# Performance work log

Measured on AMD Instinct MI355X. Metric: run time of the kernel, lower is better.

Reference implementation:

```python
import jax, jax.numpy as jnp
import numpy as np

B, S, D, H, FF = 2, 4096, 1024, 16, 4096
HD = D // H


def _layernorm(x, g, b, eps=1e-5):
    mu = jnp.mean(x, axis=-1, keepdims=True)
    var = jnp.var(x, axis=-1, keepdims=True)
    return (x - mu) * jax.lax.rsqrt(var + eps) * g + b


def setup_inputs() -> dict:
    key = jax.random.key(0)
    ks = jax.random.split(key, 20)
    sd = 1.0 / np.sqrt(D)
    sf = 1.0 / np.sqrt(FF)
    inp = {
        "x": jax.random.normal(ks[0], (B, S, D), jnp.float32),
        # attention projections, stored as [in, out]
        "wq": jax.random.normal(ks[1], (D, D), jnp.float32) * sd,
        "bq": jnp.zeros((D,), jnp.float32),
        "wk": jax.random.normal(ks[2], (D, D), jnp.float32) * sd,
        "bk": jnp.zeros((D,), jnp.float32),
        "wv": jax.random.normal(ks[3], (D, D), jnp.float32) * sd,
        "bv": jnp.zeros((D,), jnp.float32),
        "wo": jax.random.normal(ks[4], (D, D), jnp.float32) * sd,
        "bo": jnp.zeros((D,), jnp.float32),
        # block norm1 (pre-attention)
        "ln1_g": jnp.ones((D,), jnp.float32),
        "ln1_b": jnp.zeros((D,), jnp.float32),
        # FFN internal norm
        "lnf_g": jnp.ones((D,), jnp.float32),
        "lnf_b": jnp.zeros((D,), jnp.float32),
        # gated FFN
        "w1": jax.random.normal(ks[5], (D, FF), jnp.float32) * sd,
        "b1": jnp.zeros((FF,), jnp.float32),
        "wg": jax.random.normal(ks[6], (D, FF), jnp.float32) * sd,
        "bg": jnp.zeros((FF,), jnp.float32),
        "w2": jax.random.normal(ks[7], (FF, D), jnp.float32) * sf,
        "b2": jnp.zeros((D,), jnp.float32),
    }
    return inp


def reference(x, wq, bq, wk, bk, wv, bv, wo, bo, ln1_g, ln1_b,
              lnf_g, lnf_b, w1, b1, wg, bg, w2, b2):
    # pre-norm attention
    residual = x
    h = _layernorm(x, ln1_g, ln1_b)
    q = (h @ wq + bq).reshape(B, S, H, HD).transpose(0, 2, 1, 3)  # [B,H,S,hd]
    k = (h @ wk + bk).reshape(B, S, H, HD).transpose(0, 2, 1, 3)
    v = (h @ wv + bv).reshape(B, S, H, HD).transpose(0, 2, 1, 3)
    scores = jnp.einsum("bhqd,bhkd->bhqk", q, k) / np.sqrt(HD)
    attn = jax.nn.softmax(scores, axis=-1)  # [B,H,S,S] materialized as in torch src
    ctx = jnp.einsum("bhqk,bhkd->bhqd", attn, v)
    ctx = ctx.transpose(0, 2, 1, 3).reshape(B, S, D)
    attn_out = ctx @ wo + bo
    x = residual + attn_out  # dropout = 0 (eval)

    # gated FFN with internal pre-norm and residual
    res2 = x
    h2 = _layernorm(x, lnf_g, lnf_b)
    gate = jax.nn.sigmoid(h2 @ wg + bg)
    up = jax.nn.gelu(h2 @ w1 + b1, approximate=False)
    out = (up * gate) @ w2 + b2
    return out + res2
```

## Files before the change

### kernel.cpp

```cpp
#include <hip/hip_runtime.h>
#include <hip/hip_bf16.h>

#define BB 2
#define SS 4096
#define DD 1024
#define HH 16
#define HD 64
#define FF 4096
#define MM (BB*SS)

typedef __hip_bfloat16 bf16;
typedef __attribute__((ext_vector_type(8))) __bf16 v8bf;
typedef __attribute__((ext_vector_type(4))) float f32x4;
typedef __attribute__((ext_vector_type(16))) float f32x16;
typedef __attribute__((ext_vector_type(8))) unsigned short u16v8;

__device__ __forceinline__ f32x4 mfma16(v8bf a, v8bf b, f32x4 c) {
  return __builtin_amdgcn_mfma_f32_16x16x32_bf16(a, b, c, 0, 0, 0);
}
__device__ __forceinline__ f32x16 mfma32(v8bf a, v8bf b, f32x16 c) {
  return __builtin_amdgcn_mfma_f32_32x32x16_bf16(a, b, c, 0, 0, 0);
}
__device__ __forceinline__ void gload16(const void* g, void* l) {
  __builtin_amdgcn_global_load_lds((const __attribute__((address_space(1))) void*)g,
                                   (__attribute__((address_space(3))) void*)l, 16, 0, 0);
}
__device__ __forceinline__ unsigned cvtpk_bf16(float lo, float hi) {
  unsigned r;
  asm("v_cvt_pk_bf16_f32 %0, %1, %2" : "=v"(r) : "v"(lo), "v"(hi));
  return r;
}

__global__ void k_tcvt(const float* __restrict__ W, bf16* __restrict__ Wt, int K, int N)
{
  __shared__ float tile[32][33];
  const int n0 = blockIdx.x * 32, k0 = blockIdx.y * 32;
  const int tx = threadIdx.x, ty = threadIdx.y;
#pragma unroll
  for (int i = 0; i < 32; i += 8)
    tile[ty + i][tx] = W[(long)(k0 + ty + i) * N + n0 + tx];
  __syncthreads();
#pragma unroll
  for (int i = 0; i < 32; i += 8)
    Wt[(long)(n0 + ty + i) * K + k0 + tx] = __float2bfloat16(tile[tx][ty + i]);
}

__global__ __launch_bounds__(256)
void k_vtrans(const bf16* __restrict__ V, bf16* __restrict__ Vt)
{
  __shared__ bf16 tile[64][72];
  const int s0 = blockIdx.x * 64;
  const int h  = blockIdx.y;
  const int b  = blockIdx.z;
  const int t  = threadIdx.x;
  const int r = t >> 3, c8 = t & 7;
#pragma unroll
  for (int it = 0; it < 2; ++it) {
    const int sr = it * 32 + r;
    const u16v8 v = *(const u16v8*)(V + (long)(b * SS + s0 + sr) * DD + h * 64 + c8 * 8);
#pragma unroll
    for (int e = 0; e < 8; ++e)
      ((unsigned short*)&tile[sr][0])[c8 * 8 + e] = v[e];
  }
  __syncthreads();
#pragma unroll
  for (int it = 0; it < 2; ++it) {
    const int d = it * 32 + r;
    union { unsigned short s[8]; u16v8 v; } o;
#pragma unroll
    for (int e = 0; e < 8; ++e)
      o.s[e] = ((const unsigned short*)tile)[(c8 * 8 + e) * 72 + d];
    *(u16v8*)(Vt + ((long)(b * HH + h) * HD + d) * (long)SS + s0 + c8 * 8) = o.v;
  }
}

__global__ __launch_bounds__(256)
void k_layernorm(const float* __restrict__ x, const float* __restrict__ g,
                 const float* __restrict__ b, bf16* __restrict__ out)
{
  const int row = blockIdx.x;
  const float4 v = ((const float4*)(x + (long)row * DD))[threadIdx.x];
  float s  = v.x + v.y + v.z + v.w;
  float s2 = v.x*v.x + v.y*v.y + v.z*v.z + v.w*v.w;
#pragma unroll
  for (int off = 1; off < 64; off <<= 1) {
    s  += __shfl_xor(s,  off);
    s2 += __shfl_xor(s2, off);
  }
  __shared__ float red[8];
  if ((threadIdx.x & 63) == 0) {
    red[threadIdx.x >> 6]       = s;
    red[(threadIdx.x >> 6) + 4] = s2;
  }
  __syncthreads();
  s  = red[0] + red[1] + red[2] + red[3];
  s2 = red[4] + red[5] + red[6] + red[7];
  const float mu = s * (1.f / DD);
  const float rs = rsqrtf(s2 * (1.f / DD) - mu * mu + 1e-5f);
  const float4 gv = ((const float4*)g)[threadIdx.x];
  const float4 bv = ((const float4*)b)[threadIdx.x];
  bf16* op = out + (long)row * DD + threadIdx.x * 4;
  op[0] = __float2bfloat16((v.x - mu) * rs * gv.x + bv.x);
  op[1] = __float2bfloat16((v.y - mu) * rs * gv.y + bv.y);
  op[2] = __float2bfloat16((v.z - mu) * rs * gv.z + bv.z);
  op[3] = __float2bfloat16((v.w - mu) * rs * gv.w + bv.w);
}

template<int EPI>
__global__ __launch_bounds__(256, 2)
void k_gemm(const bf16* __restrict__ A, const bf16* __restrict__ Bt,
            const float* __restrict__ bias, const float* __restrict__ res,
            void* __restrict__ Cout, int M, int N, int K, float scale)
{
  __shared__ __align__(16) bf16 As[128 * 32];
  __shared__ __align__(16) bf16 Bs[128 * 32];
  const int t = threadIdx.x;
  const int lane = t & 63, w = t >> 6;
  const int wr = w >> 1, wc = w & 1;
  const int fr = lane & 15, fq = lane >> 4;
  const long m0 = (long)blockIdx.y * 128, n0 = (long)blockIdx.x * 128;

  f32x4 acc[4][4] = {};

  const bf16* Ag0 = A  + (m0 + (t >> 2)) * K + (t & 3) * 8;
  const bf16* Ag1 = Ag0 + 64L * K;
  const bf16* Bg0 = Bt + (n0 + (t >> 2)) * K + (t & 3) * 8;
  const bf16* Bg1 = Bg0 + 64L * K;
  bf16* Al0 = As + t * 8;
  bf16* Al1 = As + 2048 + t * 8;
  bf16* Bl0 = Bs + t * 8;
  bf16* Bl1 = Bs + 2048 + t * 8;

  for (int kk = 0; kk < K; kk += 32) {
    gload16(Ag0 + kk, Al0);
    gload16(Ag1 + kk, Al1);
    gload16(Bg0 + kk, Bl0);
    gload16(Bg1 + kk, Bl1);
    __syncthreads();
    v8bf af[4], bfr[4];
#pragma unroll
    for (int mt = 0; mt < 4; ++mt)
      af[mt] = *(const v8bf*)&As[(wr*64 + mt*16 + fr) * 32 + fq*8];
#pragma unroll
    for (int nt = 0; nt < 4; ++nt)
      bfr[nt] = *(const v8bf*)&Bs[(wc*64 + nt*16 + fr) * 32 + fq*8];
#pragma unroll
    for (int mt = 0; mt < 4; ++mt)
#pragma unroll
      for (int nt = 0; nt < 4; ++nt)
        acc[mt][nt] = mfma16(af[mt], bfr[nt], acc[mt][nt]);
    __syncthreads();
  }

#pragma unroll
  for (int nt = 0; nt < 4; ++nt) {
    const long col = n0 + wc*64 + nt*16 + fr;
    const float bv = bias[col];
#pragma unroll
    for (int mt = 0; mt < 4; ++mt) {
#pragma unroll
      for (int j = 0; j < 4; ++j) {
        const long row = m0 + wr*64 + mt*16 + fq*4 + j;
        float v = (acc[mt][nt][j] + bv) * scale;
        if (EPI == 0) {
          ((bf16*)Cout)[row * N + col] = __float2bfloat16(v);
        } else {
          ((float*)Cout)[row * N + col] = v + res[row * N + col];
        }
      }
    }
  }
}

__global__ __launch_bounds__(256, 2)
void k_ffn_dual(const bf16* __restrict__ A, const bf16* __restrict__ BgT,
                const bf16* __restrict__ BuT, const float* __restrict__ bgb,
                const float* __restrict__ bub, bf16* __restrict__ Out)
{
  __shared__ __align__(16) bf16 As[128 * 32];
  __shared__ __align__(16) bf16 Gs[128 * 32];
  __shared__ __align__(16) bf16 Us[128 * 32];
  const int t = threadIdx.x;
  const int lane = t & 63, w = t >> 6;
  const int wr = w >> 1, wc = w & 1;
  const int fr = lane & 15, fq = lane >> 4;
  const long m0 = (long)blockIdx.y * 128, n0 = (long)blockIdx.x * 128;
  const int K = DD;

  f32x4 ag[4][4] = {}, au[4][4] = {};

  const bf16* Ag0 = A   + (m0 + (t >> 2)) * K + (t & 3) * 8;
  const bf16* Ag1 = Ag0 + 64L * K;
  const bf16* Gg0 = BgT + (n0 + (t >> 2)) * K + (t & 3) * 8;
  const bf16* Gg1 = Gg0 + 64L * K;
  const bf16* Ug0 = BuT + (n0 + (t >> 2)) * K + (t & 3) * 8;
  const bf16* Ug1 = Ug0 + 64L * K;

  for (int kk = 0; kk < K; kk += 32) {
    gload16(Ag0 + kk, As + t * 8);
    gload16(Ag1 + kk, As + 2048 + t * 8);
    gload16(Gg0 + kk, Gs + t * 8);
    gload16(Gg1 + kk, Gs + 2048 + t * 8);
    gload16(Ug0 + kk, Us + t * 8);
    gload16(Ug1 + kk, Us + 2048 + t * 8);
    __syncthreads();
    v8bf af[4], gf[4], uf[4];
#pragma unroll
    for (int mt = 0; mt < 4; ++mt)
      af[mt] = *(const v8bf*)&As[(wr*64 + mt*16 + fr) * 32 + fq*8];
#pragma unroll
    for (int nt = 0; nt < 4; ++nt) {
      gf[nt] = *(const v8bf*)&Gs[(wc*64 + nt*16 + fr) * 32 + fq*8];
      uf[nt] = *(const v8bf*)&Us[(wc*64 + nt*16 + fr) * 32 + fq*8];
    }
#pragma unroll
    for (int mt = 0; mt < 4; ++mt)
#pragma unroll
      for (int nt = 0; nt < 4; ++nt) {
        ag[mt][nt] = mfma16(af[mt], gf[nt], ag[mt][nt]);
        au[mt][nt] = mfma16(af[mt], uf[nt], au[mt][nt]);
      }
    __syncthreads();
  }

#pragma unroll
  for (int nt = 0; nt < 4; ++nt) {
    const long col = n0 + wc*64 + nt*16 + fr;
    const float gb = bgb[col], ub = bub[col];
#pragma unroll
    for (int mt = 0; mt < 4; ++mt) {
#pragma unroll
      for (int j = 0; j < 4; ++j) {
        const long row = m0 + wr*64 + mt*16 + fq*4 + j;
        const float g = ag[mt][nt][j] + gb;
        const float u = au[mt][nt][j] + ub;
        const float sg = 1.f / (1.f + __expf(-g));
        const float gl = 0.5f * u * (1.f + erff(u * 0.70710678118f));
        Out[row * FF + col] = __float2bfloat16(sg * gl);
      }
    }
  }
}

__global__ __launch_bounds__(256, 2)
void k_attn(const bf16* __restrict__ Qb, const bf16* __restrict__ Kb,
            const bf16* __restrict__ Vt, bf16* __restrict__ ctx)
{
  __shared__ __align__(16) bf16 Ksh[2][4096];
  __shared__ __align__(16) bf16 Vsh[2][4096];
  const int t = threadIdx.x;
  const int lane = t & 63, w = t >> 6;
  const int q5 = lane & 31, hi = lane >> 5;
  const int q0 = blockIdx.x * 128;
  const int h = blockIdx.y, b = blockIdx.z;
  const long qk_base = ((long)b * SS) * DD + h * HD;
  const long vt_base = ((long)(b * HH + h)) * ((long)HD * SS);

  const int r0 = t >> 3;
  const int cswz = ((t & 7) * 16) ^ ((r0 & 7) << 4);
  const bf16* kg = Kb + qk_base + (long)r0 * DD + (cswz >> 1);
  const bf16* vg = Vt + vt_base + (long)r0 * SS + (cswz >> 1);

  v8bf qf[4];
  {
    const bf16* qp = Qb + qk_base + (long)(q0 + w * 32 + q5) * DD + hi * 8;
#pragma unroll
    for (int c = 0; c < 4; ++c) qf[c] = *(const v8bf*)(qp + c * 16);
  }

  int kcol[4];
#pragma unroll
  for (int c = 0; c < 4; ++c)
    kcol[c] = ((c * 32 + hi * 16) ^ ((q5 & 7) << 4)) >> 1;

  float m_ = -1e30f, l_ = 0.f;
  f32x16 o0 = {}, o1 = {};

#define STAGE(bufidx, kv0_) do {                                  \
    const bf16* kp_ = kg + (long)(kv0_) * DD;                     \
    gload16(kp_,            &Ksh[bufidx][t * 8]);                 \
    gload16(kp_ + 32L * DD, &Ksh[bufidx][2048 + t * 8]);          \
    const bf16* vp_ = vg + (kv0_);                                \
    gload16(vp_,            &Vsh[bufidx][t * 8]);                 \
    gload16(vp_ + 32L * SS, &Vsh[bufidx][2048 + t * 8]);          \
  } while (0)

  STAGE(0, 0);
  __syncthreads();

  for (int tt = 0; tt < SS / 64; ++tt) {
    const int cur = tt & 1;
    if (tt + 1 < SS / 64) STAGE(cur ^ 1, (tt + 1) * 64);

    f32x16 s0 = {}, s1 = {};
#pragma unroll
    for (int c = 0; c < 4; ++c) {
      const v8bf k0 = *(const v8bf*)&Ksh[cur][q5 * 64 + kcol[c]];
      const v8bf k1 = *(const v8bf*)&Ksh[cur][(32 + q5) * 64 + kcol[c]];
      s0 = mfma32(k0, qf[c], s0);
      s1 = mfma32(k1, qf[c], s1);
    }

    float pm = s0[0];
#pragma unroll
    for (int r = 1; r < 16; ++r) pm = fmaxf(pm, s0[r]);
#pragma unroll
    for (int r = 0; r < 16; ++r) pm = fmaxf(pm, s1[r]);
    pm = fmaxf(pm, __shfl_xor(pm, 32));
    const float mn = fmaxf(m_, pm);
    const float al = __builtin_amdgcn_exp2f(m_ - mn);
    m_ = mn;
    float rs = 0.f;
#pragma unroll
    for (int r = 0; r < 16; ++r) { s0[r] = __builtin_amdgcn_exp2f(s0[r] - mn); rs += s0[r]; }
#pragma unroll
    for (int r = 0; r < 16; ++r) { s1[r] = __builtin_amdgcn_exp2f(s1[r] - mn); rs += s1[r]; }
    rs += __shfl_xor(rs, 32);
    l_ = l_ * al + rs;
#pragma unroll
    for (int r = 0; r < 16; ++r) { o0[r] *= al; o1[r] *= al; }

    v8bf pb[4];
#pragma unroll
    for (int c = 0; c < 4; ++c) {
      const int base = (c & 1) * 8;
      unsigned wa0, wa1, wb0, wb1;
      if (c < 2) {
        wa0 = cvtpk_bf16(s0[base + 0], s0[base + 1]);
        wa1 = cvtpk_bf16(s0[base + 2], s0[base + 3]);
        wb0 = cvtpk_bf16(s0[base + 4], s0[base + 5]);
        wb1 = cvtpk_bf16(s0[base + 6], s0[base + 7]);
      } else {
        wa0 = cvtpk_bf16(s1[base + 0], s1[base + 1]);
        wa1 = cvtpk_bf16(s1[base + 2], s1[base + 3]);
        wb0 = cvtpk_bf16(s1[base + 4], s1[base + 5]);
        wb1 = cvtpk_bf16(s1[base + 6], s1[base + 7]);
      }
      asm("v_permlane32_swap_b32 %0, %1" : "+v"(wa0), "+v"(wb0));
      asm("v_permlane32_swap_b32 %0, %1" : "+v"(wa1), "+v"(wb1));
      union { unsigned u[4]; v8bf v; } cvt;
      cvt.u[0] = wa0; cvt.u[1] = wa1; cvt.u[2] = wb0; cvt.u[3] = wb1;
      pb[c] = cvt.v;
    }

#pragma unroll
    for (int c = 0; c < 4; ++c) {
      const v8bf v0f = *(const v8bf*)&Vsh[cur][q5 * 64 + kcol[c]];
      const v8bf v1f = *(const v8bf*)&Vsh[cur][(32 + q5) * 64 + kcol[c]];
      o0 = mfma32(v0f, pb[c], o0);
      o1 = mfma32(v1f, pb[c], o1);
    }
    __syncthreads();
  }
#undef STAGE

  const float inv = 1.f / l_;
  bf16* Osh = &Ksh[0][0];
  const int qrow = w * 32 + q5;
  const int oswz = (qrow & 7) << 4;
#pragma unroll
  for (int r = 0; r < 16; ++r) {
    const int d0 = (r & 3) + 8 * (r >> 2) + 4 * hi;
    Osh[((qrow * 128 + d0 * 2) ^ oswz) >> 1]        = __float2bfloat16(o0[r] * inv);
    Osh[((qrow * 128 + (32 + d0) * 2) ^ oswz) >> 1] = __float2bfloat16(o1[r] * inv);
  }
  __syncthreads();
  {
    const int q = t >> 1, half = t & 1;
    const int qs = (q & 7) << 4;
    bf16* cp = ctx + qk_base + (long)(q0 + q) * DD + half * 32;
#pragma unroll
    for (int s = 0; s < 4; ++s) {
      const int byte = (q * 128 + half * 64 + s * 16) ^ qs;
      *(u16v8*)(cp + s * 8) = *(const u16v8*)&Osh[byte >> 1];
    }
  }
}

extern "C" void kernel_launch(void* const* d_in, const int* in_sizes, int n_in,
                              void* d_out, int out_size, void* d_ws, size_t ws_size,
                              hipStream_t stream)
{
  const float* x    = (const float*)d_in[0];
  const float* wq   = (const float*)d_in[1];
  const float* bq   = (const float*)d_in[2];
  const float* wk   = (const float*)d_in[3];
  const float* bk   = (const float*)d_in[4];
  const float* wv   = (const float*)d_in[5];
  const float* bv   = (const float*)d_in[6];
  const float* wo   = (const float*)d_in[7];
  const float* bo   = (const float*)d_in[8];
  const float* ln1g = (const float*)d_in[9];
  const float* ln1b = (const float*)d_in[10];
  const float* lnfg = (const float*)d_in[11];
  const float* lnfb = (const float*)d_in[12];
  const float* w1   = (const float*)d_in[13];
  const float* b1   = (const float*)d_in[14];
  const float* wg   = (const float*)d_in[15];
  const float* bg   = (const float*)d_in[16];
  const float* w2   = (const float*)d_in[17];
  const float* b2   = (const float*)d_in[18];

  char* ws = (char*)d_ws;
  const size_t MB = 1u << 20;
  bf16*  WqT  = (bf16*)(ws + 0 * MB);
  bf16*  WkT  = (bf16*)(ws + 2 * MB);
  bf16*  WvT  = (bf16*)(ws + 4 * MB);
  bf16*  WoT  = (bf16*)(ws + 6 * MB);
  bf16*  W1T  = (bf16*)(ws + 8 * MB);
  bf16*  WgT  = (bf16*)(ws + 16 * MB);
  bf16*  W2T  = (bf16*)(ws + 24 * MB);
  float* x1   = (float*)(ws + 32 * MB);
  bf16*  hbuf = (bf16*)(ws + 64 * MB);
  bf16*  Qb   = (bf16*)(ws + 80 * MB);
  bf16*  Kb   = (bf16*)(ws + 96 * MB);
  bf16*  Vb   = (bf16*)(ws + 112 * MB);
  bf16*  Vtb  = (bf16*)(ws + 128 * MB);
  bf16*  ctxb = hbuf;
  bf16*  prod = (bf16*)(ws + 80 * MB);

  dim3 tb(32, 8);
  k_tcvt<<<dim3(32, 32), tb, 0, stream>>>(wq, WqT, 1024, 1024);
  k_tcvt<<<dim3(32, 32), tb, 0, stream>>>(wk, WkT, 1024, 1024);
  k_tcvt<<<dim3(32, 32), tb, 0, stream>>>(wv, WvT, 1024, 1024);
  k_tcvt<<<dim3(32, 32), tb, 0, stream>>>(wo, WoT, 1024, 1024);
  k_tcvt<<<dim3(128, 32), tb, 0, stream>>>(w1, W1T, 1024, 4096);
  k_tcvt<<<dim3(128, 32), tb, 0, stream>>>(wg, WgT, 1024, 4096);
  k_tcvt<<<dim3(32, 128), tb, 0, stream>>>(w2, W2T, 4096, 1024);

  k_layernorm<<<MM, 256, 0, stream>>>(x, ln1g, ln1b, hbuf);

  const float qscale = 0.1803368801111204f;
  dim3 g1(1024 / 128, MM / 128);
  k_gemm<0><<<g1, 256, 0, stream>>>(hbuf, WqT, bq, nullptr, Qb, MM, 1024, 1024, qscale);
  k_gemm<0><<<g1, 256, 0, stream>>>(hbuf, WkT, bk, nullptr, Kb, MM, 1024, 1024, 1.f);
  k_gemm<0><<<g1, 256, 0, stream>>>(hbuf, WvT, bv, nullptr, Vb, MM, 1024, 1024, 1.f);
  k_vtrans<<<dim3(SS / 64, HH, BB), 256, 0, stream>>>(Vb, Vtb);

  k_attn<<<dim3(SS / 128, HH, BB), 256, 0, stream>>>(Qb, Kb, Vtb, ctxb);

  k_gemm<1><<<g1, 256, 0, stream>>>(ctxb, WoT, bo, x, x1, MM, 1024, 1024, 1.f);

  k_layernorm<<<MM, 256, 0, stream>>>(x1, lnfg, lnfb, hbuf);

  k_ffn_dual<<<dim3(FF / 128, MM / 128), 256, 0, stream>>>(hbuf, WgT, W1T, bg, b1, prod);

  k_gemm<1><<<g1, 256, 0, stream>>>(prod, W2T, b2, x1, (float*)d_out, MM, 1024, 4096, 1.f);
}
```

Before: 659.8 us.

## Interleave gate/up FFN weights into one matrix and pair columns within a tile

The gate and up weight matrices are transposed into a single interleaved buffer, in alternating 64-row chunks. The dual-B FFN kernel becomes a single-B GEMM over 2*FF columns: one half of the waves computes gate and the other computes up for the same 64 output columns. The up values pass through swizzled LDS to the gate waves, which apply sigmoid*gelu and write the product. This halves per-block accumulator and LDS usage, which may allow higher occupancy. In exchange, half the waves sit idle in the epilogue, the block count doubles, and up is rounded to bf16 before GELU.

```diff
diff --git a/kernel.cpp b/kernel.cpp
--- a/kernel.cpp
+++ b/kernel.cpp
@@ -31,7 +31,8 @@
   return r;
 }
 
-__global__ void k_tcvt(const float* __restrict__ W, bf16* __restrict__ Wt, int K, int N)
+__global__ void k_tcvt(const float* __restrict__ W, bf16* __restrict__ Wt, int K, int N,
+                       int pairsel)
 {
   __shared__ float tile[32][33];
   const int n0 = blockIdx.x * 32, k0 = blockIdx.y * 32;
@@ -41,8 +42,11 @@
     tile[ty + i][tx] = W[(long)(k0 + ty + i) * N + n0 + tx];
   __syncthreads();
 #pragma unroll
-  for (int i = 0; i < 32; i += 8)
-    Wt[(long)(n0 + ty + i) * K + k0 + tx] = __float2bfloat16(tile[tx][ty + i]);
+  for (int i = 0; i < 32; i += 8) {
+    long orow = n0 + ty + i;
+    if (pairsel >= 0) orow = ((orow >> 6) << 7) + pairsel * 64 + (orow & 63);
+    Wt[orow * K + k0 + tx] = __float2bfloat16(tile[tx][ty + i]);
+  }
 }
 
 __global__ __launch_bounds__(256)
@@ -173,71 +177,82 @@
 }
 
 __global__ __launch_bounds__(256, 2)
-void k_ffn_dual(const bf16* __restrict__ A, const bf16* __restrict__ BgT,
-                const bf16* __restrict__ BuT, const float* __restrict__ bgb,
-                const float* __restrict__ bub, bf16* __restrict__ Out)
-{
-  __shared__ __align__(16) bf16 As[128 * 32];
-  __shared__ __align__(16) bf16 Gs[128 * 32];
-  __shared__ __align__(16) bf16 Us[128 * 32];
+void k_ffn_pair(const bf16* __restrict__ A, const bf16* __restrict__ WguT,
+                const float* __restrict__ bgb, const float* __restrict__ bub,
+                bf16* __restrict__ Out)
+{
+  __shared__ __align__(16) bf16 smem[8192];
+  bf16* As = smem;
+  bf16* Bs = smem + 4096;
   const int t = threadIdx.x;
   const int lane = t & 63, w = t >> 6;
   const int wr = w >> 1, wc = w & 1;
   const int fr = lane & 15, fq = lane >> 4;
   const long m0 = (long)blockIdx.y * 128, n0 = (long)blockIdx.x * 128;
+  const int tc0 = blockIdx.x * 64;
   const int K = DD;
 
-  f32x4 ag[4][4] = {}, au[4][4] = {};
-
-  const bf16* Ag0 = A   + (m0 + (t >> 2)) * K + (t & 3) * 8;
-  const bf16* Ag1 = Ag0 + 64L * K;
-  const bf16* Gg0 = BgT + (n0 + (t >> 2)) * K + (t & 3) * 8;
-  const bf16* Gg1 = Gg0 + 64L * K;
-  const bf16* Ug0 = BuT + (n0 + (t >> 2)) * K + (t & 3) * 8;
-  const bf16* Ug1 = Ug0 + 64L * K;
+  f32x4 acc[4][4] = {};
+
+  const bf16* Ag0 = A    + (m0 + (t >> 2)) * K + (t & 3) * 8;
+  const bf16* Ag1 = Ag0  + 64L * K;
+  const bf16* Bg0 = WguT + (n0 + (t >> 2)) * K + (t & 3) * 8;
+  const bf16* Bg1 = Bg0  + 64L * K;
 
   for (int kk = 0; kk < K; kk += 32) {
     gload16(Ag0 + kk, As + t * 8);
     gload16(Ag1 + kk, As + 2048 + t * 8);
-    gload16(Gg0 + kk, Gs + t * 8);
-    gload16(Gg1 + kk, Gs + 2048 + t * 8);
-    gload16(Ug0 + kk, Us + t * 8);
-    gload16(Ug1 + kk, Us + 2048 + t * 8);
+    gload16(Bg0 + kk, Bs + t * 8);
+    gload16(Bg1 + kk, Bs + 2048 + t * 8);
     __syncthreads();
-    v8bf af[4], gf[4], uf[4];
+    v8bf af[4], bfr[4];
 #pragma unroll
     for (int mt = 0; mt < 4; ++mt)
       af[mt] = *(const v8bf*)&As[(wr*64 + mt*16 + fr) * 32 + fq*8];
 #pragma unroll
+    for (int nt = 0; nt < 4; ++nt)
+      bfr[nt] = *(const v8bf*)&Bs[(wc*64 + nt*16 + fr) * 32 + fq*8];
+#pragma unroll
+    for (int mt = 0; mt < 4; ++mt)
+#pragma unroll
+      for (int nt = 0; nt < 4; ++nt)
+        acc[mt][nt] = mfma16(af[mt], bfr[nt], acc[mt][nt]);
+    __syncthreads();
+  }
+
+  if (wc == 1) {
+#pragma unroll
     for (int nt = 0; nt < 4; ++nt) {
-      gf[nt] = *(const v8bf*)&Gs[(wc*64 + nt*16 + fr) * 32 + fq*8];
-      uf[nt] = *(const v8bf*)&Us[(wc*64 + nt*16 + fr) * 32 + fq*8];
-    }
-#pragma unroll
-    for (int mt = 0; mt < 4; ++mt)
-#pragma unroll
-      for (int nt = 0; nt < 4; ++nt) {
-        ag[mt][nt] = mfma16(af[mt], gf[nt], ag[mt][nt]);
-        au[mt][nt] = mfma16(af[mt], uf[nt], au[mt][nt]);
-      }
-    __syncthreads();
-  }
-
-#pragma unroll
-  for (int nt = 0; nt < 4; ++nt) {
-    const long col = n0 + wc*64 + nt*16 + fr;
-    const float gb = bgb[col], ub = bub[col];
-#pragma unroll
-    for (int mt = 0; mt < 4; ++mt) {
-#pragma unroll
-      for (int j = 0; j < 4; ++j) {
-        const long row = m0 + wr*64 + mt*16 + fq*4 + j;
-        const float g = ag[mt][nt][j] + gb;
-        const float u = au[mt][nt][j] + ub;
-        const float sg = 1.f / (1.f + __expf(-g));
-        const float gl = 0.5f * u * (1.f + erff(u * 0.70710678118f));
-        Out[row * FF + col] = __float2bfloat16(sg * gl);
-      }
+      const int c = nt*16 + fr;
+      const float ub = bub[tc0 + c];
+#pragma unroll
+      for (int mt = 0; mt < 4; ++mt)
+#pragma unroll
+        for (int j = 0; j < 4; ++j) {
+          const int lrow = wr*64 + mt*16 + fq*4 + j;
+          smem[lrow*64 + (c ^ (((lrow >> 2) & 3) << 4))] =
+              __float2bfloat16(acc[mt][nt][j] + ub);
+        }
+    }
+  }
+  __syncthreads();
+  if (wc == 0) {
+#pragma unroll
+    for (int nt = 0; nt < 4; ++nt) {
+      const int c = nt*16 + fr;
+      const float gb = bgb[tc0 + c];
+#pragma unroll
+      for (int mt = 0; mt < 4; ++mt)
+#pragma unroll
+        for (int j = 0; j < 4; ++j) {
+          const int lrow = wr*64 + mt*16 + fq*4 + j;
+          const float g = acc[mt][nt][j] + gb;
+          const float u =
+              __bfloat162float(smem[lrow*64 + (c ^ (((lrow >> 2) & 3) << 4))]);
+          const float sg = 1.f / (1.f + __expf(-g));
+          const float gl = 0.5f * u * (1.f + erff(u * 0.70710678118f));
+          Out[(m0 + lrow) * FF + tc0 + c] = __float2bfloat16(sg * gl);
+        }
     }
   }
 }
@@ -407,8 +422,7 @@
   bf16*  WkT  = (bf16*)(ws + 2 * MB);
   bf16*  WvT  = (bf16*)(ws + 4 * MB);
   bf16*  WoT  = (bf16*)(ws + 6 * MB);
-  bf16*  W1T  = (bf16*)(ws + 8 * MB);
-  bf16*  WgT  = (bf16*)(ws + 16 * MB);
+  bf16*  WguT = (bf16*)(ws + 8 * MB);
   bf16*  W2T  = (bf16*)(ws + 24 * MB);
   float* x1   = (float*)(ws + 32 * MB);
   bf16*  hbuf = (bf16*)(ws + 64 * MB);
@@ -420,13 +434,13 @@
   bf16*  prod = (bf16*)(ws + 80 * MB);
 
   dim3 tb(32, 8);
-  k_tcvt<<<dim3(32, 32), tb, 0, stream>>>(wq, WqT, 1024, 1024);
-  k_tcvt<<<dim3(32, 32), tb, 0, stream>>>(wk, WkT, 1024, 1024);
-  k_tcvt<<<dim3(32, 32), tb, 0, stream>>>(wv, WvT, 1024, 1024);
-  k_tcvt<<<dim3(32, 32), tb, 0, stream>>>(wo, WoT, 1024, 1024);
-  k_tcvt<<<dim3(128, 32), tb, 0, stream>>>(w1, W1T, 1024, 4096);
-  k_tcvt<<<dim3(128, 32), tb, 0, stream>>>(wg, WgT, 1024, 4096);
-  k_tcvt<<<dim3(32, 128), tb, 0, stream>>>(w2, W2T, 4096, 1024);
+  k_tcvt<<<dim3(32, 32), tb, 0, stream>>>(wq, WqT, 1024, 1024, -1);
+  k_tcvt<<<dim3(32, 32), tb, 0, stream>>>(wk, WkT, 1024, 1024, -1);
+  k_tcvt<<<dim3(32, 32), tb, 0, stream>>>(wv, WvT, 1024, 1024, -1);
+  k_tcvt<<<dim3(32, 32), tb, 0, stream>>>(wo, WoT, 1024, 1024, -1);
+  k_tcvt<<<dim3(128, 32), tb, 0, stream>>>(wg, WguT, 1024, 4096, 0);
+  k_tcvt<<<dim3(128, 32), tb, 0, stream>>>(w1, WguT, 1024, 4096, 1);
+  k_tcvt<<<dim3(32, 128), tb, 0, stream>>>(w2, W2T, 4096, 1024, -1);
 
   k_layernorm<<<MM, 256, 0, stream>>>(x, ln1g, ln1b, hbuf);
 
@@ -443,7 +457,7 @@
 
   k_layernorm<<<MM, 256, 0, stream>>>(x1, lnfg, lnfb, hbuf);
 
-  k_ffn_dual<<<dim3(FF / 128, MM / 128), 256, 0, stream>>>(hbuf, WgT, W1T, bg, b1, prod);
+  k_ffn_pair<<<dim3(2 * FF / 128, MM / 128), 256, 0, stream>>>(hbuf, WguT, bg, b1, prod);
 
   k_gemm<1><<<g1, 256, 0, stream>>>(prod, W2T, b2, x1, (float*)d_out, MM, 1024, 4096, 1.f);
 }
```

Measured after the change: 656.2 us. About the same (-0.5%).

## Add XCD-aware block remapping and shrink FFN dual GEMM N-tile

Applied to the files above, without the earlier changes.

Adds a block-index swizzle that spreads consecutive workgroups across the eight XCDs in the GEMM, dual-FFN and attention kernels, so tiles sharing operands land on the same L2. The dual FFN GEMM tile drops from 128x128 to 128x64, halving accumulator registers and LDS, which may raise occupancy, at the cost of reloading the A tile twice as often. It also adds an unused scale parameter to the weight conversion kernel and makes small cosmetic cleanups.

```diff
diff --git a/kernel.cpp b/kernel.cpp
--- a/kernel.cpp
+++ b/kernel.cpp
@@ -30,8 +30,16 @@
   asm("v_cvt_pk_bf16_f32 %0, %1, %2" : "=v"(r) : "v"(lo), "v"(hi));
   return r;
 }
-
-__global__ void k_tcvt(const float* __restrict__ W, bf16* __restrict__ Wt, int K, int N)
+__device__ __forceinline__ void xcd_swz(int& bx, int& by) {
+  const int nwg = gridDim.x * gridDim.y;
+  int o = blockIdx.y * gridDim.x + blockIdx.x;
+  o = (o & 7) * (nwg >> 3) + (o >> 3);
+  bx = o % gridDim.x;
+  by = o / gridDim.x;
+}
+
+__global__ void k_tcvt(const float* __restrict__ W, bf16* __restrict__ Wt, int K, int N,
+                       float scale)
 {
   __shared__ float tile[32][33];
   const int n0 = blockIdx.x * 32, k0 = blockIdx.y * 32;
@@ -42,7 +50,7 @@
   __syncthreads();
 #pragma unroll
   for (int i = 0; i < 32; i += 8)
-    Wt[(long)(n0 + ty + i) * K + k0 + tx] = __float2bfloat16(tile[tx][ty + i]);
+    Wt[(long)(n0 + ty + i) * K + k0 + tx] = __float2bfloat16(tile[tx][ty + i] * scale);
 }
 
 __global__ __launch_bounds__(256)
@@ -114,11 +122,13 @@
 {
   __shared__ __align__(16) bf16 As[128 * 32];
   __shared__ __align__(16) bf16 Bs[128 * 32];
+  int bx, by;
+  xcd_swz(bx, by);
   const int t = threadIdx.x;
   const int lane = t & 63, w = t >> 6;
   const int wr = w >> 1, wc = w & 1;
   const int fr = lane & 15, fq = lane >> 4;
-  const long m0 = (long)blockIdx.y * 128, n0 = (long)blockIdx.x * 128;
+  const long m0 = (long)by * 128, n0 = (long)bx * 128;
 
   f32x4 acc[4][4] = {};
 
@@ -126,16 +136,12 @@
   const bf16* Ag1 = Ag0 + 64L * K;
   const bf16* Bg0 = Bt + (n0 + (t >> 2)) * K + (t & 3) * 8;
   const bf16* Bg1 = Bg0 + 64L * K;
-  bf16* Al0 = As + t * 8;
-  bf16* Al1 = As + 2048 + t * 8;
-  bf16* Bl0 = Bs + t * 8;
-  bf16* Bl1 = Bs + 2048 + t * 8;
 
   for (int kk = 0; kk < K; kk += 32) {
-    gload16(Ag0 + kk, Al0);
-    gload16(Ag1 + kk, Al1);
-    gload16(Bg0 + kk, Bl0);
-    gload16(Bg1 + kk, Bl1);
+    gload16(Ag0 + kk, As + t * 8);
+    gload16(Ag1 + kk, As + 2048 + t * 8);
+    gload16(Bg0 + kk, Bs + t * 8);
+    gload16(Bg1 + kk, Bs + 2048 + t * 8);
     __syncthreads();
     v8bf af[4], bfr[4];
 #pragma unroll
@@ -162,11 +168,8 @@
       for (int j = 0; j < 4; ++j) {
         const long row = m0 + wr*64 + mt*16 + fq*4 + j;
         float v = (acc[mt][nt][j] + bv) * scale;
-        if (EPI == 0) {
-          ((bf16*)Cout)[row * N + col] = __float2bfloat16(v);
-        } else {
-          ((float*)Cout)[row * N + col] = v + res[row * N + col];
-        }
+        if (EPI == 0) ((bf16*)Cout)[row * N + col] = __float2bfloat16(v);
+        else          ((float*)Cout)[row * N + col] = v + res[row * N + col];
       }
     }
   }
@@ -178,45 +181,43 @@
                 const float* __restrict__ bub, bf16* __restrict__ Out)
 {
   __shared__ __align__(16) bf16 As[128 * 32];
-  __shared__ __align__(16) bf16 Gs[128 * 32];
-  __shared__ __align__(16) bf16 Us[128 * 32];
+  __shared__ __align__(16) bf16 Gs[64 * 32];
+  __shared__ __align__(16) bf16 Us[64 * 32];
+  int bx, by;
+  xcd_swz(bx, by);
   const int t = threadIdx.x;
   const int lane = t & 63, w = t >> 6;
   const int wr = w >> 1, wc = w & 1;
   const int fr = lane & 15, fq = lane >> 4;
-  const long m0 = (long)blockIdx.y * 128, n0 = (long)blockIdx.x * 128;
+  const long m0 = (long)by * 128, n0 = (long)bx * 64;
   const int K = DD;
 
-  f32x4 ag[4][4] = {}, au[4][4] = {};
+  f32x4 ag[4][2] = {}, au[4][2] = {};
 
   const bf16* Ag0 = A   + (m0 + (t >> 2)) * K + (t & 3) * 8;
   const bf16* Ag1 = Ag0 + 64L * K;
-  const bf16* Gg0 = BgT + (n0 + (t >> 2)) * K + (t & 3) * 8;
-  const bf16* Gg1 = Gg0 + 64L * K;
-  const bf16* Ug0 = BuT + (n0 + (t >> 2)) * K + (t & 3) * 8;
-  const bf16* Ug1 = Ug0 + 64L * K;
+  const bf16* Gg  = BgT + (n0 + (t >> 2)) * K + (t & 3) * 8;
+  const bf16* Ug  = BuT + (n0 + (t >> 2)) * K + (t & 3) * 8;
 
   for (int kk = 0; kk < K; kk += 32) {
     gload16(Ag0 + kk, As + t * 8);
     gload16(Ag1 + kk, As + 2048 + t * 8);
-    gload16(Gg0 + kk, Gs + t * 8);
-    gload16(Gg1 + kk, Gs + 2048 + t * 8);
-    gload16(Ug0 + kk, Us + t * 8);
-    gload16(Ug1 + kk, Us + 2048 + t * 8);
+    gload16(Gg + kk, Gs + t * 8);
+    gload16(Ug + kk, Us + t * 8);
     __syncthreads();
-    v8bf af[4], gf[4], uf[4];
+    v8bf af[4], gf[2], uf[2];
 #pragma unroll
     for (int mt = 0; mt < 4; ++mt)
       af[mt] = *(const v8bf*)&As[(wr*64 + mt*16 + fr) * 32 + fq*8];
 #pragma unroll
-    for (int nt = 0; nt < 4; ++nt) {
-      gf[nt] = *(const v8bf*)&Gs[(wc*64 + nt*16 + fr) * 32 + fq*8];
-      uf[nt] = *(const v8bf*)&Us[(wc*64 + nt*16 + fr) * 32 + fq*8];
+    for (int nt = 0; nt < 2; ++nt) {
+      gf[nt] = *(const v8bf*)&Gs[(wc*32 + nt*16 + fr) * 32 + fq*8];
+      uf[nt] = *(const v8bf*)&Us[(wc*32 + nt*16 + fr) * 32 + fq*8];
     }
 #pragma unroll
     for (int mt = 0; mt < 4; ++mt)
 #pragma unroll
-      for (int nt = 0; nt < 4; ++nt) {
+      for (int nt = 0; nt < 2; ++nt) {
         ag[mt][nt] = mfma16(af[mt], gf[nt], ag[mt][nt]);
         au[mt][nt] = mfma16(af[mt], uf[nt], au[mt][nt]);
       }
@@ -224,8 +225,8 @@
   }
 
 #pragma unroll
-  for (int nt = 0; nt < 4; ++nt) {
-    const long col = n0 + wc*64 + nt*16 + fr;
+  for (int nt = 0; nt < 2; ++nt) {
+    const long col = n0 + wc*32 + nt*16 + fr;
     const float gb = bgb[col], ub = bub[col];
 #pragma unroll
     for (int mt = 0; mt < 4; ++mt) {
@@ -251,8 +252,12 @@
   const int t = threadIdx.x;
   const int lane = t & 63, w = t >> 6;
   const int q5 = lane & 31, hi = lane >> 5;
-  const int q0 = blockIdx.x * 128;
-  const int h = blockIdx.y, b = blockIdx.z;
+
+  int o = blockIdx.x + 32 * (blockIdx.y + 16 * blockIdx.z);
+  o = (o & 7) * 128 + (o >> 3);
+  const int q0 = (o & 31) * 128;
+  const int h = (o >> 5) & 15, b = o >> 9;
+
   const long qk_base = ((long)b * SS) * DD + h * HD;
   const long vt_base = ((long)(b * HH + h)) * ((long)HD * SS);
 
@@ -419,18 +424,19 @@
   bf16*  ctxb = hbuf;
   bf16*  prod = (bf16*)(ws + 80 * MB);
 
+  const float qscale = 0.1803368801111204f;
+
   dim3 tb(32, 8);
-  k_tcvt<<<dim3(32, 32), tb, 0, stream>>>(wq, WqT, 1024, 1024);
-  k_tcvt<<<dim3(32, 32), tb, 0, stream>>>(wk, WkT, 1024, 1024);
-  k_tcvt<<<dim3(32, 32), tb, 0, stream>>>(wv, WvT, 1024, 1024);
-  k_tcvt<<<dim3(32, 32), tb, 0, stream>>>(wo, WoT, 1024, 1024);
-  k_tcvt<<<dim3(128, 32), tb, 0, stream>>>(w1, W1T, 1024, 4096);
-  k_tcvt<<<dim3(128, 32), tb, 0, stream>>>(wg, WgT, 1024, 4096);
-  k_tcvt<<<dim3(32, 128), tb, 0, stream>>>(w2, W2T, 4096, 1024);
+  k_tcvt<<<dim3(32, 32), tb, 0, stream>>>(wq, WqT, 1024, 1024, 1.f);
+  k_tcvt<<<dim3(32, 32), tb, 0, stream>>>(wk, WkT, 1024, 1024, 1.f);
+  k_tcvt<<<dim3(32, 32), tb, 0, stream>>>(wv, WvT, 1024, 1024, 1.f);
+  k_tcvt<<<dim3(32, 32), tb, 0, stream>>>(wo, WoT, 1024, 1024, 1.f);
+  k_tcvt<<<dim3(128, 32), tb, 0, stream>>>(w1, W1T, 1024, 4096, 1.f);
+  k_tcvt<<<dim3(128, 32), tb, 0, stream>>>(wg, WgT, 1024, 4096, 1.f);
+  k_tcvt<<<dim3(32, 128), tb, 0, stream>>>(w2, W2T, 4096, 1024, 1.f);
 
   k_layernorm<<<MM, 256, 0, stream>>>(x, ln1g, ln1b, hbuf);
 
-  const float qscale = 0.1803368801111204f;
   dim3 g1(1024 / 128, MM / 128);
   k_gemm<0><<<g1, 256, 0, stream>>>(hbuf, WqT, bq, nullptr, Qb, MM, 1024, 1024, qscale);
   k_gemm<0><<<g1, 256, 0, stream>>>(hbuf, WkT, bk, nullptr, Kb, MM, 1024, 1024, 1.f);
@@ -443,7 +449,7 @@
 
   k_layernorm<<<MM, 256, 0, stream>>>(x1, lnfg, lnfb, hbuf);
 
-  k_ffn_dual<<<dim3(FF / 128, MM / 128), 256, 0, stream>>>(hbuf, WgT, W1T, bg, b1, prod);
+  k_ffn_dual<<<dim3(FF / 64, MM / 128), 256, 0, stream>>>(hbuf, WgT, W1T, bg, b1, prod);
 
   k_gemm<1><<<g1, 256, 0, stream>>>(prod, W2T, b2, x1, (float*)d_out, MM, 1024, 4096, 1.f);
 }
```

Measured after the change: 630.1 us. 4.5% less time.
